# Optimization experiments

Measured on AMD Instinct MI355X. Metric: run time of the kernel, lower is better.

## Reference

```python
import jax, jax.numpy as jnp
import numpy as np

NEG_SLOPE = 0.01  # nn.LeakyReLU default


def conv3x3(x, w, b):
    # x: [B,C,H,W], w: [O,I,3,3], stride 1, pad 1
    y = jax.lax.conv_general_dilated(x, w, (1, 1), 'SAME',
                                     dimension_numbers=('NCHW', 'OIHW', 'NCHW'))
    return y + b[None, :, None, None]


def bilinear_gather(img, ys, xs):
    # img: [B,C,H,W]; ys, xs: [B,K,H,W] float sample coords -> [B,C,K,H,W]
    B, C, H, W = img.shape
    imgf = img.reshape(B, C, H * W)
    y0 = jnp.floor(ys)
    x0 = jnp.floor(xs)
    out = jnp.zeros((B, C) + ys.shape[1:], img.dtype)
    for dy in (0, 1):
        for dx in (0, 1):
            yc = y0 + dy
            xc = x0 + dx
            wgt = (1.0 - jnp.abs(ys - yc)) * (1.0 - jnp.abs(xs - xc))
            valid = (yc >= 0) & (yc <= H - 1) & (xc >= 0) & (xc <= W - 1)
            wgt = jnp.where(valid, wgt, 0.0)
            idx = (jnp.clip(yc, 0, H - 1) * W + jnp.clip(xc, 0, W - 1)).astype(jnp.int32)
            g = jax.vmap(lambda f, i: f[:, i])(imgf, idx)  # [B,C,K,H,W]
            out = out + wgt[:, None] * g
    return out


def dcn_v2(x, off_feat, w_off, b_off, w, b):
    # Modulated deformable 3x3 conv (DCNv2Pack, extra_offset_mask=True, dg=1).
    B, C, H, W = x.shape
    om = conv3x3(off_feat, w_off, b_off)            # [B, 27, H, W]
    o1, o2, m = jnp.split(om, 3, axis=1)            # each [B, 9, H, W]
    off = jnp.concatenate([o1, o2], axis=1)         # [B, 18, H, W]
    off_y = off[:, 0::2]                            # [B, 9, H, W]
    off_x = off[:, 1::2]
    mask = jax.nn.sigmoid(m)                        # [B, 9, H, W]
    k = jnp.arange(3, dtype=x.dtype) - 1.0
    ky = jnp.repeat(k, 3)                           # row-major kernel order
    kx = jnp.tile(k, 3)
    hh = jnp.arange(H, dtype=x.dtype)[:, None]
    ww = jnp.arange(W, dtype=x.dtype)[None, :]
    ys = hh[None, None] + ky[None, :, None, None] + off_y
    xs = ww[None, None] + kx[None, :, None, None] + off_x
    sampled = bilinear_gather(x, ys, xs)            # [B,C,9,H,W]
    wk = w.reshape(w.shape[0], C, 9)
    out = jnp.einsum('oik,bkhw,bikhw->bohw', wk, mask, sampled)
    return out + b[None, :, None, None]


def setup_inputs() -> dict:
    key = jax.random.key(0)
    ks = jax.random.split(key, 12)
    B, C, OC, H, W = 4, 64, 32, 128, 128
    s = 0.02
    return {
        'input': jax.random.normal(ks[0], (B, C, H, W), jnp.float32),
        'offset': jax.random.normal(ks[1], (B, OC, H, W), jnp.float32),
        'w_off1': jax.random.normal(ks[2], (27, OC, 3, 3), jnp.float32) * s,
        'b_off1': jnp.zeros((27,), jnp.float32),
        'w1': jax.random.normal(ks[3], (C, C, 3, 3), jnp.float32) * s,
        'b1': jnp.zeros((C,), jnp.float32),
        'w_off2': jax.random.normal(ks[4], (27, OC, 3, 3), jnp.float32) * s,
        'b_off2': jnp.zeros((27,), jnp.float32),
        'w2': jax.random.normal(ks[5], (C, C, 3, 3), jnp.float32) * s,
        'b2': jnp.zeros((C,), jnp.float32),
        'w_last': jax.random.normal(ks[6], (C, C, 3, 3), jnp.float32) * s,
        'b_last': jnp.zeros((C,), jnp.float32),
    }


def reference(input, offset, w_off1, b_off1, w1, b1,
              w_off2, b_off2, w2, b2, w_last, b_last):
    x = dcn_v2(input, offset, w_off1, b_off1, w1, b1)
    x = jnp.where(x >= 0, x, NEG_SLOPE * x)
    out = dcn_v2(x, offset, w_off2, b_off2, w2, b2) + input
    return conv3x3(out, w_last, b_last)
```

## Files before the change

kernel.cpp:

```cpp
#include <hip/hip_runtime.h>
#include <cmath>

#define HW   16384
#define Wd   128
#define Hd   128
#define NB   4

typedef __attribute__((ext_vector_type(8))) _Float16 h16x8;
typedef __attribute__((ext_vector_type(4))) float f32x4;
typedef __attribute__((ext_vector_type(4))) unsigned int u32x4;

__device__ inline unsigned short f2h(float f) {
    _Float16 h = (_Float16)f;
    return __builtin_bit_cast(unsigned short, h);
}
__device__ inline _Float16 u2h(unsigned short u) {
    return __builtin_bit_cast(_Float16, u);
}

__device__ inline void repack_one(int idx, const float* __restrict__ s1, const float* __restrict__ s2,
                                  int Osplit, int O, int CIN, int KS, unsigned short* __restrict__ dst) {
    int e    = idx & 7;
    int lane = (idx >> 3) & 63;
    int ks   = (idx >> 9) % KS;
    int m    = (idx / (512 * KS)) & 3;
    int k    = idx / (2048 * KS);
    int oc = m * 16 + (lane & 15);
    int c  = ks * 32 + (lane >> 4) * 8 + e;
    float v = 0.f;
    if (oc < O && c < CIN)
        v = (oc < Osplit) ? s1[((size_t)oc * CIN + c) * 9 + k]
                          : s2[((size_t)(oc - Osplit) * CIN + c) * 9 + k];
    dst[idx] = f2h(v);
}

__global__ __launch_bounds__(256) void prep(
    const float* __restrict__ input, const float* __restrict__ offset,
    const float* __restrict__ w_off1, const float* __restrict__ w_off2,
    const float* __restrict__ b_off1, const float* __restrict__ b_off2,
    const float* __restrict__ w1, const float* __restrict__ w2, const float* __restrict__ w_last,
    unsigned short* __restrict__ xn, unsigned short* __restrict__ offn,
    unsigned short* __restrict__ wfo, unsigned short* __restrict__ wf1,
    unsigned short* __restrict__ wf2, unsigned short* __restrict__ wfl,
    float* __restrict__ bias54)
{
    int blk = blockIdx.x;
    if (blk < 512) {
        int t = blk * 256 + threadIdx.x;
        if (t < 65536) {
            int b = t >> 14, p = t & 16383;
            const float* s = input + ((size_t)b * 64) * HW + p;
            unsigned short* d = xn + (size_t)t * 64;
#pragma unroll
            for (int g = 0; g < 8; g++) {
                unsigned short pk[8];
#pragma unroll
                for (int e = 0; e < 8; e++) pk[e] = f2h(s[(size_t)(g * 8 + e) * HW]);
                *(u32x4*)(d + g * 8) = *(u32x4*)pk;
            }
        } else {
            int u = t - 65536;
            int b = u >> 14, p = u & 16383;
            const float* s = offset + ((size_t)b * 32) * HW + p;
            unsigned short* d = offn + (size_t)u * 32;
#pragma unroll
            for (int g = 0; g < 4; g++) {
                unsigned short pk[8];
#pragma unroll
                for (int e = 0; e < 8; e++) pk[e] = f2h(s[(size_t)(g * 8 + e) * HW]);
                *(u32x4*)(d + g * 8) = *(u32x4*)pk;
            }
        }
    } else {
        int u = (blk - 512) * 256 + threadIdx.x;
        if (u < 18432)        repack_one(u, w_off1, w_off1, 27, 27, 32, 1, wfo);
        else if (u < 36864)   repack_one(u - 18432, w_off2, w_off2, 27, 27, 32, 1, wfo + 18432);
        else if (u < 73728)   repack_one(u - 36864, w1, w1, 64, 64, 64, 2, wf1);
        else if (u < 110592)  repack_one(u - 73728, w2, w2, 64, 64, 64, 2, wf2);
        else if (u < 147456)  repack_one(u - 110592, w_last, w_last, 64, 64, 64, 2, wfl);
        else if (u < 147510) {
            int j = u - 147456;
            bias54[j] = (j < 27) ? b_off1[j] : b_off2[j - 27];
        }
    }
}

__global__ __launch_bounds__(512, 8) void conv_stage64(
    const unsigned short* __restrict__ xn, const unsigned short* __restrict__ wf,
    const float* __restrict__ bias, float* __restrict__ out)
{
    __shared__ __align__(16) unsigned short stage[198 * 64];
    int lb = ((blockIdx.x & 7) << 7) | (blockIdx.x >> 3);
    int t = threadIdx.x;
    int pxbase = lb * 64;
    int b = pxbase >> 14;
    int pbase = pxbase & 16383;
    int rowbase = pbase >> 7, colbase = pbase & 127;
    const unsigned short* xb = xn + ((size_t)(b << 14)) * 64;

    for (int q = t; q < 1584; q += 512) {
        int ps = q >> 3, j = q & 7;
        int ly = ps / 66, lx = ps - ly * 66;
        int y = rowbase - 1 + ly, x = colbase - 1 + lx;
        bool ok = (y >= 0) & (y < Hd) & (x >= 0) & (x < Wd);
        u32x4 v = {0, 0, 0, 0};
        if (ok) v = *(const u32x4*)(xb + ((size_t)(y * Wd + x)) * 64 + j * 8);
        *(u32x4*)(stage + ps * 64 + ((j ^ (ps & 7)) << 3)) = v;
    }
    __syncthreads();

    int lane = t & 63;
    int wave = t >> 6;
    int kh = wave >> 2;
    int wv = wave & 3;
    int sp = wv * 16 + (lane & 15);
    int px = pxbase + sp;
    int p = px & 16383;
    int cg = lane >> 4;
    int cch = kh * 4 + cg;

    const h16x8* wfv = (const h16x8*)wf;
    f32x4 acc[4];
#pragma unroll
    for (int m = 0; m < 4; m++) acc[m] = (f32x4){0.f, 0.f, 0.f, 0.f};

#pragma unroll
    for (int k = 0; k < 9; k++) {
        int ps = (k / 3) * 66 + sp + (k % 3);
        h16x8 bq = *(const h16x8*)(stage + ps * 64 + ((cch ^ (ps & 7)) << 3));
        h16x8 aF[4];
#pragma unroll
        for (int m = 0; m < 4; m++)
            aF[m] = wfv[((k * 4 + m) * 2 + kh) * 64 + lane];
#pragma unroll
        for (int m = 0; m < 4; m++)
            acc[m] = __builtin_amdgcn_mfma_f32_16x16x32_f16(aF[m], bq, acc[m], 0, 0, 0);
    }

    __syncthreads();
    float* red = (float*)stage;
    if (kh == 1) {
#pragma unroll
        for (int m = 0; m < 4; m++)
#pragma unroll
            for (int j = 0; j < 4; j++)
                red[(m * 4 + j) * 256 + wv * 64 + lane] = acc[m][j];
    }
    __syncthreads();
    if (kh == 0) {
#pragma unroll
        for (int m = 0; m < 4; m++) {
            int ocb = m * 16 + cg * 4;
#pragma unroll
            for (int r = 0; r < 4; r++) {
                int oc = ocb + r;
                float v = acc[m][r] + red[(m * 4 + r) * 256 + wv * 64 + lane] + bias[oc];
                out[((size_t)b * 64 + oc) * HW + p] = v;
            }
        }
    }
}

struct Tap { float w00, w01, w10, w11; int o00, o01, o10, o11; };

__device__ inline Tap mkparams(float oy, float ox, float mv, int row, int col, int k) {
    Tap P;
    float mk = 1.f / (1.f + __expf(-mv));
    float ys = (float)(row + k / 3 - 1) + oy;
    float xs = (float)(col + k % 3 - 1) + ox;
    float y0f = floorf(ys), x0f = floorf(xs);
    float fy = ys - y0f, fx = xs - x0f;
    int y0 = (int)y0f, x0 = (int)x0f;
    int y1 = y0 + 1, x1 = x0 + 1;
    bool vy0 = (y0 >= 0) & (y0 < Hd);
    bool vy1 = (y1 >= 0) & (y1 < Hd);
    bool vx0 = (x0 >= 0) & (x0 < Wd);
    bool vx1 = (x1 >= 0) & (x1 < Wd);
    P.w00 = (vy0 && vx0) ? (1.f - fy) * (1.f - fx) * mk : 0.f;
    P.w01 = (vy0 && vx1) ? (1.f - fy) * fx * mk : 0.f;
    P.w10 = (vy1 && vx0) ? fy * (1.f - fx) * mk : 0.f;
    P.w11 = (vy1 && vx1) ? fy * fx * mk : 0.f;
    int iy0 = min(max(y0, 0), Hd - 1) * Wd;
    int iy1 = min(max(y1, 0), Hd - 1) * Wd;
    int ix0 = min(max(x0, 0), Wd - 1);
    int ix1 = min(max(x1, 0), Wd - 1);
    P.o00 = iy0 + ix0; P.o01 = iy0 + ix1; P.o10 = iy1 + ix0; P.o11 = iy1 + ix1;
    return P;
}

template<int EPI>
__global__ __launch_bounds__(512, 4) void dcn_fused(
    const unsigned short* __restrict__ xn, const unsigned short* __restrict__ offn,
    const unsigned short* __restrict__ wfo, const float* __restrict__ obias,
    const unsigned short* __restrict__ wf, const float* __restrict__ bias,
    const float* __restrict__ resid, unsigned short* __restrict__ outn)
{
    __shared__ __align__(16) unsigned short stage[490 * 64];
    __shared__ unsigned twp0[576], twp1[576];
    __shared__ unsigned tap0[576], tap1[576];

    unsigned short* offstage = stage;
    float* omt = (float*)(stage + 6336);

    int lb = ((blockIdx.x & 7) << 7) | (blockIdx.x >> 3);
    int t = threadIdx.x;
    int pxbase = lb * 64;
    int b = pxbase >> 14;
    int pbase = pxbase & 16383;
    int rowbase = pbase >> 7;
    int colbase = pbase & 127;
    int ybase = rowbase - 3;
    int xbase = colbase - 3;
    const unsigned short* xb = xn + ((size_t)(b << 14)) * 64;
    const unsigned short* ob = offn + ((size_t)(b << 14)) * 32;

    for (int q = t; q < 792; q += 512) {
        int ps = q >> 2, j = q & 3;
        int ly = ps / 66, lx = ps - ly * 66;
        int y = rowbase - 1 + ly, x = colbase - 1 + lx;
        bool ok = (y >= 0) & (y < Hd) & (x >= 0) & (x < Wd);
        u32x4 v = {0, 0, 0, 0};
        if (ok) v = *(const u32x4*)(ob + ((size_t)(y * Wd + x)) * 32 + j * 8);
        *(u32x4*)(offstage + ps * 32 + ((j ^ (ps & 3)) << 3)) = v;
    }
    __syncthreads();

    int lane = t & 63;
    int wave = t >> 6;

    if (wave < 4) {
        int osp = wave * 16 + (lane & 15);
        int cg4 = lane >> 4;
        const h16x8* wfv = (const h16x8*)wfo;
        f32x4 oacc[2];
#pragma unroll
        for (int m = 0; m < 2; m++) oacc[m] = (f32x4){0.f, 0.f, 0.f, 0.f};
#pragma unroll
        for (int k = 0; k < 9; k++) {
            int ps = (k / 3) * 66 + osp + (k % 3);
            h16x8 bq = *(const h16x8*)(offstage + ps * 32 + ((cg4 ^ (ps & 3)) << 3));
#pragma unroll
            for (int m = 0; m < 2; m++) {
                h16x8 aF = wfv[(k * 4 + m) * 64 + lane];
                oacc[m] = __builtin_amdgcn_mfma_f32_16x16x32_f16(aF, bq, oacc[m], 0, 0, 0);
            }
        }
#pragma unroll
        for (int m = 0; m < 2; m++) {
            int ocb = m * 16 + cg4 * 4;
#pragma unroll
            for (int r = 0; r < 4; r++) {
                int oc = ocb + r;
                if (oc < 27) omt[oc * 64 + osp] = oacc[m][r] + obias[oc];
            }
        }
    }
    __syncthreads();

    for (int s = t; s < 576; s += 512) {
        int k = s >> 6, sp2 = s & 63;
        int row = rowbase, col = colbase + sp2;
        float oy = omt[(2 * k) * 64 + sp2];
        float ox = omt[(2 * k + 1) * 64 + sp2];
        float mv = omt[(18 + k) * 64 + sp2];
        Tap P = mkparams(oy, ox, mv, row, col, k);

        unsigned a[4];
        int oo[4] = {P.o00, P.o01, P.o10, P.o11};
#pragma unroll
        for (int c = 0; c < 4; c++) {
            int o = oo[c];
            int y = o >> 7, x = o & 127;
            int ly = y - ybase, lx = x - xbase;
            bool inw = ((unsigned)ly < 7u) & ((unsigned)lx < 70u);
            int ps = min(max(ly, 0), 6) * 70 + min(max(lx, 0), 69);
            a[c] = inw ? (unsigned)((ps << 3) | (ps & 7)) : (0x8000u | (unsigned)o);
        }
        twp0[s] = (unsigned)f2h(P.w00) | ((unsigned)f2h(P.w01) << 16);
        twp1[s] = (unsigned)f2h(P.w10) | ((unsigned)f2h(P.w11) << 16);
        tap0[s] = a[0] | (a[1] << 16);
        tap1[s] = a[2] | (a[3] << 16);
    }
    __syncthreads();

    for (int q = t; q < 3920; q += 512) {
        int ps = q >> 3, j = q & 7;
        int ly = ps / 70, lx = ps - ly * 70;
        int y = min(max(ybase + ly, 0), Hd - 1);
        int x = min(max(xbase + lx, 0), Wd - 1);
        u32x4 v = *(const u32x4*)(xb + ((size_t)(y * Wd + x)) * 64 + j * 8);
        *(u32x4*)(stage + ps * 64 + ((j ^ (ps & 7)) << 3)) = v;
    }
    __syncthreads();

    int kh = wave >> 2;
    int wv = wave & 3;
    int sp = wv * 16 + (lane & 15);
    int px = pxbase + sp;
    int p = px & 16383;
    int cg = lane >> 4;
    int c0 = kh * 32 + cg * 8;
    int cch = kh * 4 + cg;

    const h16x8* wfv = (const h16x8*)wf;

    f32x4 acc[4];
#pragma unroll
    for (int m = 0; m < 4; m++) acc[m] = (f32x4){0.f, 0.f, 0.f, 0.f};

#pragma unroll
    for (int k = 0; k < 9; k++) {
        int s = k * 64 + sp;
        unsigned a01 = tap0[s], a23 = tap1[s];
        unsigned w01 = twp0[s], w23 = twp1[s];

        unsigned code[4] = { a01 & 0xffffu, a01 >> 16, a23 & 0xffffu, a23 >> 16 };
        h16x8 gc[4];
#pragma unroll
        for (int c = 0; c < 4; c++)
            gc[c] = *(const h16x8*)((const char*)stage + (((code[c] & 0xFFFu) ^ (unsigned)cch) << 4));

        if (__builtin_expect((a01 | a23) & 0x80008000u, 0)) {
#pragma unroll
            for (int c = 0; c < 4; c++)
                if (code[c] & 0x8000u)
                    gc[c] = *(const h16x8*)(xb + (size_t)(code[c] & 0x7fffu) * 64 + c0);
        }

        _Float16 h00 = u2h((unsigned short)(w01 & 0xffffu));
        _Float16 h01 = u2h((unsigned short)(w01 >> 16));
        _Float16 h10 = u2h((unsigned short)(w23 & 0xffffu));
        _Float16 h11 = u2h((unsigned short)(w23 >> 16));
        h16x8 bF = gc[0] * h00;
        bF = gc[1] * h01 + bF;
        bF = gc[2] * h10 + bF;
        bF = gc[3] * h11 + bF;

        h16x8 aF[4];
#pragma unroll
        for (int m = 0; m < 4; m++)
            aF[m] = wfv[((k * 4 + m) * 2 + kh) * 64 + lane];
#pragma unroll
        for (int m = 0; m < 4; m++)
            acc[m] = __builtin_amdgcn_mfma_f32_16x16x32_f16(aF[m], bF, acc[m], 0, 0, 0);
    }

    __syncthreads();
    float* red = (float*)stage;
    if (kh == 1) {
#pragma unroll
        for (int m = 0; m < 4; m++)
#pragma unroll
            for (int j = 0; j < 4; j++)
                red[(m * 4 + j) * 256 + wv * 64 + lane] = acc[m][j];
    }
    __syncthreads();
    if (kh == 0) {
        unsigned short* drow = outn + (size_t)px * 64;
#pragma unroll
        for (int m = 0; m < 4; m++) {
            int ocb = m * 16 + cg * 4;
            unsigned short pk[4];
#pragma unroll
            for (int r = 0; r < 4; r++) {
                int oc = ocb + r;
                float v = acc[m][r] + red[(m * 4 + r) * 256 + wv * 64 + lane] + bias[oc];
                if (EPI == 0) v = (v >= 0.f) ? v : 0.01f * v;
                if (EPI == 1) v += resid[((size_t)b * 64 + oc) * HW + p];
                pk[r] = f2h(v);
            }
            *(ushort4*)(drow + ocb) = *(ushort4*)pk;
        }
    }
}

extern "C" void kernel_launch(void* const* d_in, const int* in_sizes, int n_in,
                              void* d_out, int out_size, void* d_ws, size_t ws_size,
                              hipStream_t stream)
{
    const float* input  = (const float*)d_in[0];
    const float* offset = (const float*)d_in[1];
    const float* w_off1 = (const float*)d_in[2];
    const float* b_off1 = (const float*)d_in[3];
    const float* w1     = (const float*)d_in[4];
    const float* b1     = (const float*)d_in[5];
    const float* w_off2 = (const float*)d_in[6];
    const float* b_off2 = (const float*)d_in[7];
    const float* w2     = (const float*)d_in[8];
    const float* b2     = (const float*)d_in[9];
    const float* w_last = (const float*)d_in[10];
    const float* b_last = (const float*)d_in[11];
    float* out = (float*)d_out;

    unsigned short* xn   = (unsigned short*)d_ws;
    unsigned short* offn = xn + 4194304;
    unsigned short* x1n  = offn + 2097152;
    unsigned short* x2n  = x1n + 4194304;
    unsigned short* wfo  = x2n + 4194304;
    unsigned short* wf1  = wfo + 36864;
    unsigned short* wf2  = wf1 + 36864;
    unsigned short* wfl  = wf2 + 36864;
    float* bias54 = (float*)(wfl + 36864);

    prep<<<dim3(1089), 256, 0, stream>>>(input, offset, w_off1, w_off2, b_off1, b_off2,
                                         w1, w2, w_last, xn, offn, wfo, wf1, wf2, wfl, bias54);

    dcn_fused<0><<<dim3(1024), 512, 0, stream>>>(xn, offn, wfo, bias54,
                                                 wf1, b1, nullptr, x1n);
    dcn_fused<1><<<dim3(1024), 512, 0, stream>>>(x1n, offn, wfo + 18432, bias54 + 27,
                                                 wf2, b2, input, x2n);
    conv_stage64<<<dim3(1024), 512, 0, stream>>>(x2n, wfl, b_last, out);
}
```

Baseline: 79.39 us.

## Overlap input tile staging with offset conv and tap-parameter phases

The offset/mask table moves out of the shared staging buffer into its own shared array, so loading the input tile no longer has to wait until the offset features are consumed. Input rows past the offset-feature region are now loaded in the same pass as the offset features, and the first 99 pixel slots are loaded together with the tap-parameter computation, removing a separate phase and its barrier. The offset conv is also spread over all 8 waves, one 16-channel M block each, instead of 4 waves doing two. This raises shared memory per block by about 7 KB, which may lower occupancy, and adds branch divergence inside the merged loops.

```diff
diff --git a/kernel.cpp b/kernel.cpp
--- a/kernel.cpp
+++ b/kernel.cpp
@@ -198,9 +198,9 @@
     __shared__ __align__(16) unsigned short stage[490 * 64];
     __shared__ unsigned twp0[576], twp1[576];
     __shared__ unsigned tap0[576], tap1[576];
+    __shared__ __align__(16) float omt[27 * 64];
 
     unsigned short* offstage = stage;
-    float* omt = (float*)(stage + 6336);
 
     int lb = ((blockIdx.x & 7) << 7) | (blockIdx.x >> 3);
     int t = threadIdx.x;
@@ -214,82 +214,86 @@
     const unsigned short* xb = xn + ((size_t)(b << 14)) * 64;
     const unsigned short* ob = offn + ((size_t)(b << 14)) * 32;
 
-    for (int q = t; q < 792; q += 512) {
-        int ps = q >> 2, j = q & 3;
-        int ly = ps / 66, lx = ps - ly * 66;
-        int y = rowbase - 1 + ly, x = colbase - 1 + lx;
-        bool ok = (y >= 0) & (y < Hd) & (x >= 0) & (x < Wd);
-        u32x4 v = {0, 0, 0, 0};
-        if (ok) v = *(const u32x4*)(ob + ((size_t)(y * Wd + x)) * 32 + j * 8);
-        *(u32x4*)(offstage + ps * 32 + ((j ^ (ps & 3)) << 3)) = v;
+    for (int q = t; q < 3920; q += 512) {
+        if (q < 792) {
+            int ps = q >> 2, j = q & 3;
+            int ly = ps / 66, lx = ps - ly * 66;
+            int y = rowbase - 1 + ly, x = colbase - 1 + lx;
+            bool ok = (y >= 0) & (y < Hd) & (x >= 0) & (x < Wd);
+            u32x4 v = {0, 0, 0, 0};
+            if (ok) v = *(const u32x4*)(ob + ((size_t)(y * Wd + x)) * 32 + j * 8);
+            *(u32x4*)(offstage + ps * 32 + ((j ^ (ps & 3)) << 3)) = v;
+        } else {
+            int qq = q - 792;
+            int ps = 99 + (qq >> 3), j = qq & 7;
+            int ly = ps / 70, lx = ps - ly * 70;
+            int y = min(max(ybase + ly, 0), Hd - 1);
+            int x = min(max(xbase + lx, 0), Wd - 1);
+            u32x4 v = *(const u32x4*)(xb + ((size_t)(y * Wd + x)) * 64 + j * 8);
+            *(u32x4*)(stage + ps * 64 + ((j ^ (ps & 7)) << 3)) = v;
+        }
     }
     __syncthreads();
 
     int lane = t & 63;
     int wave = t >> 6;
 
-    if (wave < 4) {
-        int osp = wave * 16 + (lane & 15);
+    {
+        int m = wave >> 2;
+        int osp = (wave & 3) * 16 + (lane & 15);
         int cg4 = lane >> 4;
-        const h16x8* wfv = (const h16x8*)wfo;
-        f32x4 oacc[2];
-#pragma unroll
-        for (int m = 0; m < 2; m++) oacc[m] = (f32x4){0.f, 0.f, 0.f, 0.f};
+        const h16x8* wfvo = (const h16x8*)wfo;
+        f32x4 oacc = (f32x4){0.f, 0.f, 0.f, 0.f};
 #pragma unroll
         for (int k = 0; k < 9; k++) {
             int ps = (k / 3) * 66 + osp + (k % 3);
             h16x8 bq = *(const h16x8*)(offstage + ps * 32 + ((cg4 ^ (ps & 3)) << 3));
-#pragma unroll
-            for (int m = 0; m < 2; m++) {
-                h16x8 aF = wfv[(k * 4 + m) * 64 + lane];
-                oacc[m] = __builtin_amdgcn_mfma_f32_16x16x32_f16(aF, bq, oacc[m], 0, 0, 0);
+            h16x8 aF = wfvo[(k * 4 + m) * 64 + lane];
+            oacc = __builtin_amdgcn_mfma_f32_16x16x32_f16(aF, bq, oacc, 0, 0, 0);
+        }
+        int ocb = m * 16 + cg4 * 4;
+#pragma unroll
+        for (int r = 0; r < 4; r++) {
+            int oc = ocb + r;
+            if (oc < 27) omt[oc * 64 + osp] = oacc[r] + obias[oc];
+        }
+    }
+    __syncthreads();
+
+    for (int q = t; q < 1368; q += 512) {
+        if (q < 576) {
+            int s = q;
+            int k = s >> 6, sp2 = s & 63;
+            int row = rowbase, col = colbase + sp2;
+            float oy = omt[(2 * k) * 64 + sp2];
+            float ox = omt[(2 * k + 1) * 64 + sp2];
+            float mv = omt[(18 + k) * 64 + sp2];
+            Tap P = mkparams(oy, ox, mv, row, col, k);
+
+            unsigned a[4];
+            int oo[4] = {P.o00, P.o01, P.o10, P.o11};
+#pragma unroll
+            for (int c = 0; c < 4; c++) {
+                int o = oo[c];
+                int y = o >> 7, x = o & 127;
+                int ly = y - ybase, lx = x - xbase;
+                bool inw = ((unsigned)ly < 7u) & ((unsigned)lx < 70u);
+                int ps = min(max(ly, 0), 6) * 70 + min(max(lx, 0), 69);
+                a[c] = inw ? (unsigned)((ps << 3) | (ps & 7)) : (0x8000u | (unsigned)o);
             }
-        }
-#pragma unroll
-        for (int m = 0; m < 2; m++) {
-            int ocb = m * 16 + cg4 * 4;
-#pragma unroll
-            for (int r = 0; r < 4; r++) {
-                int oc = ocb + r;
-                if (oc < 27) omt[oc * 64 + osp] = oacc[m][r] + obias[oc];
-            }
-        }
-    }
-    __syncthreads();
-
-    for (int s = t; s < 576; s += 512) {
-        int k = s >> 6, sp2 = s & 63;
-        int row = rowbase, col = colbase + sp2;
-        float oy = omt[(2 * k) * 64 + sp2];
-        float ox = omt[(2 * k + 1) * 64 + sp2];
-        float mv = omt[(18 + k) * 64 + sp2];
-        Tap P = mkparams(oy, ox, mv, row, col, k);
-
-        unsigned a[4];
-        int oo[4] = {P.o00, P.o01, P.o10, P.o11};
-#pragma unroll
-        for (int c = 0; c < 4; c++) {
-            int o = oo[c];
-            int y = o >> 7, x = o & 127;
-            int ly = y - ybase, lx = x - xbase;
-            bool inw = ((unsigned)ly < 7u) & ((unsigned)lx < 70u);
-            int ps = min(max(ly, 0), 6) * 70 + min(max(lx, 0), 69);
-            a[c] = inw ? (unsigned)((ps << 3) | (ps & 7)) : (0x8000u | (unsigned)o);
-        }
-        twp0[s] = (unsigned)f2h(P.w00) | ((unsigned)f2h(P.w01) << 16);
-        twp1[s] = (unsigned)f2h(P.w10) | ((unsigned)f2h(P.w11) << 16);
-        tap0[s] = a[0] | (a[1] << 16);
-        tap1[s] = a[2] | (a[3] << 16);
-    }
-    __syncthreads();
-
-    for (int q = t; q < 3920; q += 512) {
-        int ps = q >> 3, j = q & 7;
-        int ly = ps / 70, lx = ps - ly * 70;
-        int y = min(max(ybase + ly, 0), Hd - 1);
-        int x = min(max(xbase + lx, 0), Wd - 1);
-        u32x4 v = *(const u32x4*)(xb + ((size_t)(y * Wd + x)) * 64 + j * 8);
-        *(u32x4*)(stage + ps * 64 + ((j ^ (ps & 7)) << 3)) = v;
+            twp0[s] = (unsigned)f2h(P.w00) | ((unsigned)f2h(P.w01) << 16);
+            twp1[s] = (unsigned)f2h(P.w10) | ((unsigned)f2h(P.w11) << 16);
+            tap0[s] = a[0] | (a[1] << 16);
+            tap1[s] = a[2] | (a[3] << 16);
+        } else {
+            int qq = q - 576;
+            int ps = qq >> 3, j = qq & 7;
+            int ly = ps / 70, lx = ps - ly * 70;
+            int y = min(max(ybase + ly, 0), Hd - 1);
+            int x = min(max(xbase + lx, 0), Wd - 1);
+            u32x4 v = *(const u32x4*)(xb + ((size_t)(y * Wd + x)) * 64 + j * 8);
+            *(u32x4*)(stage + ps * 64 + ((j ^ (ps & 7)) << 3)) = v;
+        }
     }
     __syncthreads();
 
```

After: 80.53 us. About the same (+1.4%).
